# Kernel tuning notes

Hardware: AMD Instinct MI355X
Metric: run time of the kernel (lower is better)

The kernel has to match this reference:

```python
import jax, jax.numpy as jnp
import numpy as np

B, S, H = 4, 512, 768
D, M = 24, 96          # hdim_proj_dim, hdim_mlp_hidden
O = 2 * max(128, H // 2)  # val_mlp hidden = 768


def setup_inputs() -> dict:
    key = jax.random.key(0)
    ks = jax.random.split(key, 14)
    u = lambda k, shp, fan_in: jax.random.uniform(k, shp, jnp.float32, -1.0, 1.0) / np.float32(np.sqrt(fan_in))
    return {
        'H_j': jax.random.normal(ks[0], (B, S, H), jnp.float32),
        'H_i': jax.random.normal(ks[1], (B, S, H), jnp.float32),
        'Wpj': u(ks[2], (H, D), H),
        'Wpi': u(ks[3], (H, D), H),
        'Ws1': u(ks[4], (4 * D, M), 4 * D),
        'bs1': u(ks[5], (M,), 4 * D),
        'ws2': u(ks[6], (M,), M),
        'bs2': u(ks[7], (), M),
        'Wv1': u(ks[8], (3 * H, O), 3 * H),
        'bv1': u(ks[9], (O,), 3 * H),
        'Wv2': u(ks[10], (O, H), O),
        'bv2': u(ks[11], (H,), O),
        'alpha': jnp.float32(0.05),
        'attn_mask': jnp.ones((B, S), jnp.int32),
    }


def reference(H_j, H_i, Wpj, Wpi, Ws1, bs1, ws2, bs2, Wv1, bv1, Wv2, bv2, alpha, attn_mask):
    # Projections [B,S,D]
    Zj = H_j @ Wpj
    Zi = H_i @ Wpi
    # 4term score MLP, first layer decomposed over the concat blocks:
    # cat(Zj_p, Zi_p, Zj_p*Zi_p, |Zj_p - Zi_p|) @ Ws1
    W1j, W1i, W1h, W1d = Ws1[:D], Ws1[D:2 * D], Ws1[2 * D:3 * D], Ws1[3 * D:]
    tj = Zj @ W1j                                   # [B,P,M]
    ti = Zi @ W1i                                   # [B,Q,M]
    th = jnp.einsum('bpd,bqd,dm->bpqm', Zj, Zi, W1h)  # hadamard term
    diff = jnp.abs(Zj[:, :, None, :] - Zi[:, None, :, :])  # [B,P,Q,D]
    td = jnp.einsum('bpqd,dm->bpqm', diff, W1d)
    hid = jax.nn.relu(tj[:, :, None, :] + ti[:, None, :, :] + th + td + bs1)  # [B,P,Q,M]
    logits = jnp.einsum('bpqm,m->bpq', hid, ws2) + bs2  # [B,P,Q]
    # mask over source tokens (last dim); token_temp == 1.0 so no division
    mask = attn_mask.astype(logits.dtype)
    logits = logits + (1.0 - mask)[:, None, :] * jnp.finfo(logits.dtype).min
    probs = jax.nn.softmax(logits, axis=-1)
    ctx = jnp.einsum('bpq,bqh->bph', probs, H_i)    # [B,S,H]
    # val_mlp on cat(ctx, H_j, ctx*H_j), first layer decomposed
    Wc, Wj, Wh = Wv1[:H], Wv1[H:2 * H], Wv1[2 * H:]
    mhid = jax.nn.relu(ctx @ Wc + H_j @ Wj + (ctx * H_j) @ Wh + bv1)
    msg = mhid @ Wv2 + bv2
    # dropout is identity in eval mode
    return alpha * msg
```

## Files before the change

### kernel.cpp

```cpp
#include <hip/hip_runtime.h>
#include <hip/hip_bf16.h>

#define Bb 4
#define Ss 512
#define Hh 768
#define Dd 24
#define Mm 96
#define Oo 768

typedef __bf16 bf16x8 __attribute__((ext_vector_type(8)));
typedef float f32x4 __attribute__((ext_vector_type(4)));

__global__ __launch_bounds__(256) void proj_kernel(
    const float* __restrict__ Hj, const float* __restrict__ Hi,
    const float* __restrict__ Wpj, const float* __restrict__ Wpi,
    float* __restrict__ Zj, float* __restrict__ Zi)
{
    const int row = blockIdx.x;
    const int which = blockIdx.y;
    const float* src = (which ? Hi : Hj) + (size_t)row * Hh;
    const float* W = which ? Wpi : Wpj;
    float* Z = which ? Zi : Zj;
    __shared__ float rowbuf[Hh];
    __shared__ float partial[8][Dd];
    const int tid = threadIdx.x;
    for (int i = tid; i < Hh; i += 256) rowbuf[i] = src[i];
    __syncthreads();
    if (tid < 192) {
        const int d = tid % Dd;
        const int c = tid / Dd;
        const int h0 = c * 96;
        float s = 0.f;
        #pragma unroll 4
        for (int h = h0; h < h0 + 96; ++h) s = fmaf(rowbuf[h], W[h * Dd + d], s);
        partial[c][d] = s;
    }
    __syncthreads();
    if (tid < Dd) {
        float s = 0.f;
        #pragma unroll
        for (int c = 0; c < 8; ++c) s += partial[c][tid];
        Z[(size_t)row * Dd + tid] = s;
    }
}

__global__ __launch_bounds__(256) void transpose_bf16_kernel(
    const float* __restrict__ src, __bf16* __restrict__ dst,
    int R, int C, long sbatch, long dbatch)
{
    const float* s = src + (size_t)blockIdx.z * sbatch;
    __bf16* d = dst + (size_t)blockIdx.z * dbatch;
    __shared__ float t[32][33];
    const int x = threadIdx.x & 31, y = threadIdx.x >> 5;
    const int c0 = blockIdx.x * 32, r0 = blockIdx.y * 32;
    #pragma unroll
    for (int i = 0; i < 4; ++i)
        t[y + 8 * i][x] = s[(size_t)(r0 + y + 8 * i) * C + c0 + x];
    __syncthreads();
    #pragma unroll
    for (int i = 0; i < 4; ++i)
        d[(size_t)(c0 + y + 8 * i) * R + r0 + x] = (__bf16)t[x][y + 8 * i];
}

__global__ __launch_bounds__(256) void hjconv_kernel(
    const float* __restrict__ Hjf, __bf16* __restrict__ Ac)
{
    const int idx = blockIdx.x * 256 + threadIdx.x;
    const int row = idx / 96, c8 = idx % 96;
    const float* s = Hjf + (size_t)row * Hh + c8 * 8;
    const float4 u = *(const float4*)s;
    const float4 v = *(const float4*)(s + 4);
    bf16x8 o;
    o[0]=(__bf16)u.x; o[1]=(__bf16)u.y; o[2]=(__bf16)u.z; o[3]=(__bf16)u.w;
    o[4]=(__bf16)v.x; o[5]=(__bf16)v.y; o[6]=(__bf16)v.z; o[7]=(__bf16)v.w;
    *(bf16x8*)&Ac[(size_t)row * 2304 + Hh + c8 * 8] = o;
}

__global__ __launch_bounds__(256) void wprep_kernel(
    const float* __restrict__ Zj, const float* __restrict__ Ws1,
    const float* __restrict__ bs1, __bf16* __restrict__ Bw)
{
    __shared__ float W[96][97];
    const int tid = threadIdx.x;
    for (int i = tid; i < 96 * 96; i += 256)
        W[i / 96][i % 96] = Ws1[i];
    __syncthreads();
    const int m = tid;
    if (m >= 96) return;
    const float bs1m = bs1[m];
    for (int pp = 0; pp < 8; ++pp) {
        const int p = blockIdx.x * 8 + pp;
        const float* zr = Zj + (size_t)p * Dd;
        float tj = bs1m;
        #pragma unroll
        for (int d = 0; d < Dd; ++d) tj = fmaf(zr[d], W[d][m], tj);
        bf16x8 o[8];
        #pragma unroll
        for (int i = 0; i < 8; ++i) {
            #pragma unroll
            for (int j = 0; j < 8; ++j) {
                const int k = i * 8 + j;
                float v;
                if (k < 24)                 v = fmaf(zr[k], W[48 + k][m], W[24 + k][m]);
                else if (k == 24)           v = tj;
                else if (k >= 32 && k < 56) v = W[72 + (k - 32)][m];
                else                        v = 0.f;
                o[i][j] = (__bf16)v;
            }
        }
        __bf16* dst = Bw + (((size_t)p * 96 + m) << 6);
        #pragma unroll
        for (int i = 0; i < 8; ++i) *(bf16x8*)(dst + i * 8) = o[i];
    }
}

__global__ __launch_bounds__(256) void pair_kernel(
    const float* __restrict__ Zj, const float* __restrict__ Zi,
    const __bf16* __restrict__ Bw, const float* __restrict__ ws2,
    const float* __restrict__ bs2p, const int* __restrict__ mask,
    __bf16* __restrict__ probs)
{
    const int bp = blockIdx.x;
    const int b  = bp >> 9;
    const int tid  = threadIdx.x;
    const int lane = tid & 63;
    const int wid  = tid >> 6;
    const int col  = lane & 15;
    const int g    = lane >> 4;

    __shared__ float logitsl[Ss];
    __shared__ float red[8];

    bf16x8 aw[6][2];
    #pragma unroll
    for (int n = 0; n < 6; ++n) {
        const __bf16* base = Bw + (((size_t)bp * 96 + n * 16 + col) << 6) + g * 8;
        aw[n][0] = *(const bf16x8*)(base);
        aw[n][1] = *(const bf16x8*)(base + 32);
    }
    float ws2r[6][4];
    #pragma unroll
    for (int n = 0; n < 6; ++n) {
        const float4 w4 = *(const float4*)&ws2[n * 16 + g * 4];
        ws2r[n][0] = w4.x; ws2r[n][1] = w4.y; ws2r[n][2] = w4.z; ws2r[n][3] = w4.w;
    }

    float zj8[8];
    if (g < 3) {
        const float* zr = Zj + (size_t)bp * Dd + g * 8;
        const float4 u = *(const float4*)zr;
        const float4 v = *(const float4*)(zr + 4);
        zj8[0]=u.x; zj8[1]=u.y; zj8[2]=u.z; zj8[3]=u.w;
        zj8[4]=v.x; zj8[5]=v.y; zj8[6]=v.z; zj8[7]=v.w;
    } else {
        #pragma unroll
        for (int j = 0; j < 8; ++j) zj8[j] = 0.f;
    }

    const float* zib = Zi + (size_t)b * Ss * Dd;
    const int ko = (g < 3) ? g * 8 : 0;

    float4 cu, cv;
    {
        const float* zr = zib + (size_t)(wid * 128 + col) * Dd + ko;
        cu = *(const float4*)zr; cv = *(const float4*)(zr + 4);
    }

    for (int t = 0; t < 8; ++t) {
        const float4 u = cu, v = cv;
        if (t + 1 < 8) {
            const float* zr = zib + (size_t)(wid * 128 + (t + 1) * 16 + col) * Dd + ko;
            cu = *(const float4*)zr; cv = *(const float4*)(zr + 4);
        }
        bf16x8 b0, b1;
        if (g < 3) {
            b0[0]=(__bf16)u.x; b0[1]=(__bf16)u.y; b0[2]=(__bf16)u.z; b0[3]=(__bf16)u.w;
            b0[4]=(__bf16)v.x; b0[5]=(__bf16)v.y; b0[6]=(__bf16)v.z; b0[7]=(__bf16)v.w;
            b1[0]=(__bf16)fabsf(zj8[0]-u.x); b1[1]=(__bf16)fabsf(zj8[1]-u.y);
            b1[2]=(__bf16)fabsf(zj8[2]-u.z); b1[3]=(__bf16)fabsf(zj8[3]-u.w);
            b1[4]=(__bf16)fabsf(zj8[4]-v.x); b1[5]=(__bf16)fabsf(zj8[5]-v.y);
            b1[6]=(__bf16)fabsf(zj8[6]-v.z); b1[7]=(__bf16)fabsf(zj8[7]-v.w);
        } else {
            #pragma unroll
            for (int j = 0; j < 8; ++j) { b0[j] = (__bf16)0.f; b1[j] = (__bf16)0.f; }
            b0[0] = (__bf16)1.0f;
        }

        f32x4 acc[6];
        #pragma unroll
        for (int n = 0; n < 6; ++n) acc[n] = (f32x4){0.f, 0.f, 0.f, 0.f};
        #pragma unroll
        for (int n = 0; n < 6; ++n) {
            acc[n] = __builtin_amdgcn_mfma_f32_16x16x32_bf16(aw[n][0], b0, acc[n], 0, 0, 0);
            acc[n] = __builtin_amdgcn_mfma_f32_16x16x32_bf16(aw[n][1], b1, acc[n], 0, 0, 0);
        }

        float lsum = 0.f;
        #pragma unroll
        for (int n = 0; n < 6; ++n)
            #pragma unroll
            for (int r = 0; r < 4; ++r)
                lsum = fmaf(fmaxf(acc[n][r], 0.f), ws2r[n][r], lsum);
        lsum += __shfl_xor(lsum, 16);
        lsum += __shfl_xor(lsum, 32);
        if (lane < 16) logitsl[wid * 128 + t * 16 + lane] = lsum;
    }
    __syncthreads();

    const float bs2v = bs2p[0];
    const int* mrow = mask + (size_t)b * Ss;
    float l0 = logitsl[tid]       + bs2v + (1.0f - (float)mrow[tid])       * (-3.402823466e+38f);
    float l1 = logitsl[tid + 256] + bs2v + (1.0f - (float)mrow[tid + 256]) * (-3.402823466e+38f);
    float vmax = fmaxf(l0, l1);
    #pragma unroll
    for (int off = 32; off > 0; off >>= 1) vmax = fmaxf(vmax, __shfl_xor(vmax, off));
    if (lane == 0) red[wid] = vmax;
    __syncthreads();
    const float mx = fmaxf(fmaxf(red[0], red[1]), fmaxf(red[2], red[3]));
    const float e0 = __expf(l0 - mx);
    const float e1 = __expf(l1 - mx);
    float vs = e0 + e1;
    #pragma unroll
    for (int off = 32; off > 0; off >>= 1) vs += __shfl_xor(vs, off);
    if (lane == 0) red[4 + wid] = vs;
    __syncthreads();
    const float inv = 1.0f / (red[4] + red[5] + red[6] + red[7]);
    __bf16* prow = probs + (size_t)bp * Ss;
    prow[tid] = (__bf16)(e0 * inv);
    prow[tid + 256] = (__bf16)(e1 * inv);
}

template<int MODE>
__global__ __launch_bounds__(256) void gemm_kernel(
    const __bf16* __restrict__ A, const __bf16* __restrict__ Bt,
    const float* __restrict__ Hjf, const float* __restrict__ bias,
    const float* __restrict__ alphap,
    __bf16* __restrict__ obf, float* __restrict__ of)
{
    constexpr int K = (MODE == 0) ? 512 : (MODE == 1) ? 2304 : 768;
    constexpr int NIT = K / 64;
    constexpr int LDT = 72;

    __shared__ __bf16 As[64 * LDT];
    __shared__ __bf16 Bs[64 * LDT];

    const int tid = threadIdx.x;
    const int lane = tid & 63;
    const int wid = tid >> 6;
    const int col = lane & 15, g = lane >> 4;
    const int wm = wid >> 1, wn = wid & 1;
    const int r0 = blockIdx.x * 64;
    const int n0 = blockIdx.y * 64;
    const __bf16* Btb = (MODE == 0) ? Bt + (size_t)(r0 >> 9) * (Hh * Ss) : Bt;

    const int srow = tid >> 2;
    const int sc8  = (tid & 3) * 16;
    const __bf16* ag = A   + (size_t)(r0 + srow) * K + sc8;
    const __bf16* bg = Btb + (size_t)(n0 + srow) * K + sc8;
    __bf16* asl = &As[srow * LDT + sc8];
    __bf16* bsl = &Bs[srow * LDT + sc8];

    bf16x8 ra0 = *(const bf16x8*)(ag);
    bf16x8 ra1 = *(const bf16x8*)(ag + 8);
    bf16x8 rb0 = *(const bf16x8*)(bg);
    bf16x8 rb1 = *(const bf16x8*)(bg + 8);

    f32x4 acc[2][2];
    #pragma unroll
    for (int mi = 0; mi < 2; ++mi)
        #pragma unroll
        for (int ni = 0; ni < 2; ++ni) acc[mi][ni] = (f32x4){0.f, 0.f, 0.f, 0.f};

    for (int it = 0; it < NIT; ++it) {
        __syncthreads();
        *(bf16x8*)(asl)     = ra0;
        *(bf16x8*)(asl + 8) = ra1;
        *(bf16x8*)(bsl)     = rb0;
        *(bf16x8*)(bsl + 8) = rb1;
        __syncthreads();
        if (it + 1 < NIT) {
            const int kk = (it + 1) * 64;
            ra0 = *(const bf16x8*)(ag + kk);
            ra1 = *(const bf16x8*)(ag + kk + 8);
            rb0 = *(const bf16x8*)(bg + kk);
            rb1 = *(const bf16x8*)(bg + kk + 8);
        }
        #pragma unroll
        for (int h = 0; h < 2; ++h) {
            bf16x8 a0 = *(const bf16x8*)&As[(wm * 32 + col)      * LDT + h * 32 + g * 8];
            bf16x8 a1 = *(const bf16x8*)&As[(wm * 32 + 16 + col) * LDT + h * 32 + g * 8];
            bf16x8 b0 = *(const bf16x8*)&Bs[(wn * 32 + col)      * LDT + h * 32 + g * 8];
            bf16x8 b1 = *(const bf16x8*)&Bs[(wn * 32 + 16 + col) * LDT + h * 32 + g * 8];
            acc[0][0] = __builtin_amdgcn_mfma_f32_16x16x32_bf16(a0, b0, acc[0][0], 0, 0, 0);
            acc[0][1] = __builtin_amdgcn_mfma_f32_16x16x32_bf16(a0, b1, acc[0][1], 0, 0, 0);
            acc[1][0] = __builtin_amdgcn_mfma_f32_16x16x32_bf16(a1, b0, acc[1][0], 0, 0, 0);
            acc[1][1] = __builtin_amdgcn_mfma_f32_16x16x32_bf16(a1, b1, acc[1][1], 0, 0, 0);
        }
    }

    const float al = (MODE == 2) ? alphap[0] : 0.f;
    #pragma unroll
    for (int mi = 0; mi < 2; ++mi) {
        #pragma unroll
        for (int r = 0; r < 4; ++r) {
            const int row = r0 + wm * 32 + mi * 16 + g * 4 + r;
            #pragma unroll
            for (int ni = 0; ni < 2; ++ni) {
                const int cn = n0 + wn * 32 + ni * 16 + col;
                const float v = acc[mi][ni][r];
                if (MODE == 0) {
                    const float hjv = Hjf[(size_t)row * Hh + cn];
                    obf[(size_t)row * 2304 + cn] = (__bf16)v;
                    obf[(size_t)row * 2304 + 1536 + cn] = (__bf16)(v * hjv);
                } else if (MODE == 1) {
                    obf[(size_t)row * Oo + cn] = (__bf16)fmaxf(v + bias[cn], 0.f);
                } else {
                    of[(size_t)row * Hh + cn] = al * (v + bias[cn]);
                }
            }
        }
    }
}

extern "C" void kernel_launch(void* const* d_in, const int* in_sizes, int n_in,
                              void* d_out, int out_size, void* d_ws, size_t ws_size,
                              hipStream_t stream)
{
    const float* Hj  = (const float*)d_in[0];
    const float* Hi  = (const float*)d_in[1];
    const float* Wpj = (const float*)d_in[2];
    const float* Wpi = (const float*)d_in[3];
    const float* Ws1 = (const float*)d_in[4];
    const float* bs1 = (const float*)d_in[5];
    const float* ws2 = (const float*)d_in[6];
    const float* bs2 = (const float*)d_in[7];
    const float* Wv1 = (const float*)d_in[8];
    const float* bv1 = (const float*)d_in[9];
    const float* Wv2 = (const float*)d_in[10];
    const float* bv2 = (const float*)d_in[11];
    const float* alpha = (const float*)d_in[12];
    const int* mask  = (const int*)d_in[13];

    float* ws = (float*)d_ws;
    float* Zj = ws;
    float* Zi = Zj + 49152;
    float* R0f = Zi + 49152;
    float* R1f = R0f + 524288;
    float* Acat_f = R1f + 786432;
    float* Wv1T_f = Acat_f + 2359296;
    float* Bw_f   = Wv1T_f + 884736;

    __bf16* probs_bf = (__bf16*)R0f;
    __bf16* Wv2T     = (__bf16*)R0f;
    __bf16* HiT      = (__bf16*)R1f;
    __bf16* mhid_bf  = (__bf16*)R1f;
    __bf16* Acat     = (__bf16*)Acat_f;
    __bf16* Wv1T     = (__bf16*)Wv1T_f;
    __bf16* Bw       = (__bf16*)Bw_f;

    proj_kernel<<<dim3(Bb * Ss, 2), 256, 0, stream>>>(Hj, Hi, Wpj, Wpi, Zj, Zi);
    wprep_kernel<<<dim3(256), 256, 0, stream>>>(Zj, Ws1, bs1, Bw);
    transpose_bf16_kernel<<<dim3(Hh / 32, Ss / 32, Bb), 256, 0, stream>>>(
        Hi, HiT, Ss, Hh, (long)Ss * Hh, (long)Hh * Ss);
    transpose_bf16_kernel<<<dim3(Oo / 32, 3 * Hh / 32, 1), 256, 0, stream>>>(
        Wv1, Wv1T, 3 * Hh, Oo, 0, 0);
    hjconv_kernel<<<dim3(768), 256, 0, stream>>>(Hj, Acat);
    pair_kernel<<<dim3(Bb * Ss), 256, 0, stream>>>(Zj, Zi, Bw, ws2, bs2, mask, probs_bf);
    gemm_kernel<0><<<dim3(2048 / 64, Hh / 64), 256, 0, stream>>>(
        probs_bf, HiT, Hj, nullptr, nullptr, Acat, nullptr);
    transpose_bf16_kernel<<<dim3(Hh / 32, Oo / 32, 1), 256, 0, stream>>>(
        Wv2, Wv2T, Oo, Hh, 0, 0);
    gemm_kernel<1><<<dim3(2048 / 64, Oo / 64), 256, 0, stream>>>(
        Acat, Wv1T, nullptr, bv1, nullptr, mhid_bf, nullptr);
    gemm_kernel<2><<<dim3(2048 / 64, Hh / 64), 256, 0, stream>>>(
        mhid_bf, Wv2T, nullptr, bv2, alpha, nullptr, (float*)d_out);
}
```

Baseline: 207.1 us.

## Build pair-kernel MFMA weights in-register instead of materializing per-row Bw

Removes the wprep kernel, which wrote a per-query-row 96x64 bf16 weight tile (about 25 MB) to global memory for pair_kernel to read back. pair_kernel now builds those A operands in registers from a transposed Ws1 (new wst_kernel) and a small per-row tj table (new tj_kernel). Zi is stored padded to 32 columns, with a constant 1 in column 24 for the bias term, so the B-operand construction loses its per-lane branch. This trades a large global write and read for a few extra register FMAs per block and two tiny extra launches.

```diff
diff --git a/kernel.cpp b/kernel.cpp
--- a/kernel.cpp
+++ b/kernel.cpp
@@ -14,13 +14,12 @@
 __global__ __launch_bounds__(256) void proj_kernel(
     const float* __restrict__ Hj, const float* __restrict__ Hi,
     const float* __restrict__ Wpj, const float* __restrict__ Wpi,
-    float* __restrict__ Zj, float* __restrict__ Zi)
+    float* __restrict__ Zj, float* __restrict__ Zip)
 {
     const int row = blockIdx.x;
     const int which = blockIdx.y;
     const float* src = (which ? Hi : Hj) + (size_t)row * Hh;
     const float* W = which ? Wpi : Wpj;
-    float* Z = which ? Zi : Zj;
     __shared__ float rowbuf[Hh];
     __shared__ float partial[8][Dd];
     const int tid = threadIdx.x;
@@ -40,26 +39,33 @@
         float s = 0.f;
         #pragma unroll
         for (int c = 0; c < 8; ++c) s += partial[c][tid];
-        Z[(size_t)row * Dd + tid] = s;
-    }
-}
-
-__global__ __launch_bounds__(256) void transpose_bf16_kernel(
-    const float* __restrict__ src, __bf16* __restrict__ dst,
-    int R, int C, long sbatch, long dbatch)
-{
-    const float* s = src + (size_t)blockIdx.z * sbatch;
-    __bf16* d = dst + (size_t)blockIdx.z * dbatch;
-    __shared__ float t[32][33];
-    const int x = threadIdx.x & 31, y = threadIdx.x >> 5;
-    const int c0 = blockIdx.x * 32, r0 = blockIdx.y * 32;
-    #pragma unroll
-    for (int i = 0; i < 4; ++i)
-        t[y + 8 * i][x] = s[(size_t)(r0 + y + 8 * i) * C + c0 + x];
-    __syncthreads();
-    #pragma unroll
-    for (int i = 0; i < 4; ++i)
-        d[(size_t)(c0 + y + 8 * i) * R + r0 + x] = (__bf16)t[x][y + 8 * i];
+        if (which) Zip[(size_t)row * 32 + tid] = s;
+        else       Zj[(size_t)row * Dd + tid] = s;
+    }
+    if (which && tid >= Dd && tid < 32)
+        Zip[(size_t)row * 32 + tid] = (tid == 24) ? 1.0f : 0.0f;
+}
+
+__global__ __launch_bounds__(256) void wst_kernel(
+    const float* __restrict__ Ws1, float* __restrict__ WsT)
+{
+    __shared__ float W[96][97];
+    for (int i = threadIdx.x; i < 96 * 96; i += 256) W[i / 96][i % 96] = Ws1[i];
+    __syncthreads();
+    for (int i = threadIdx.x; i < 96 * 96; i += 256) WsT[i] = W[i % 96][i / 96];
+}
+
+__global__ __launch_bounds__(256) void tj_kernel(
+    const float* __restrict__ Zj, const float* __restrict__ Ws1,
+    const float* __restrict__ bs1, float* __restrict__ tj_all)
+{
+    const int idx = blockIdx.x * 256 + threadIdx.x;
+    const int p = idx / 96, m = idx % 96;
+    float s = bs1[m];
+    const float* zr = Zj + (size_t)p * Dd;
+    #pragma unroll
+    for (int d = 0; d < Dd; ++d) s = fmaf(zr[d], Ws1[d * Mm + m], s);
+    tj_all[idx] = s;
 }
 
 __global__ __launch_bounds__(256) void hjconv_kernel(
@@ -76,49 +82,29 @@
     *(bf16x8*)&Ac[(size_t)row * 2304 + Hh + c8 * 8] = o;
 }
 
-__global__ __launch_bounds__(256) void wprep_kernel(
-    const float* __restrict__ Zj, const float* __restrict__ Ws1,
-    const float* __restrict__ bs1, __bf16* __restrict__ Bw)
-{
-    __shared__ float W[96][97];
-    const int tid = threadIdx.x;
-    for (int i = tid; i < 96 * 96; i += 256)
-        W[i / 96][i % 96] = Ws1[i];
-    __syncthreads();
-    const int m = tid;
-    if (m >= 96) return;
-    const float bs1m = bs1[m];
-    for (int pp = 0; pp < 8; ++pp) {
-        const int p = blockIdx.x * 8 + pp;
-        const float* zr = Zj + (size_t)p * Dd;
-        float tj = bs1m;
-        #pragma unroll
-        for (int d = 0; d < Dd; ++d) tj = fmaf(zr[d], W[d][m], tj);
-        bf16x8 o[8];
-        #pragma unroll
-        for (int i = 0; i < 8; ++i) {
-            #pragma unroll
-            for (int j = 0; j < 8; ++j) {
-                const int k = i * 8 + j;
-                float v;
-                if (k < 24)                 v = fmaf(zr[k], W[48 + k][m], W[24 + k][m]);
-                else if (k == 24)           v = tj;
-                else if (k >= 32 && k < 56) v = W[72 + (k - 32)][m];
-                else                        v = 0.f;
-                o[i][j] = (__bf16)v;
-            }
-        }
-        __bf16* dst = Bw + (((size_t)p * 96 + m) << 6);
-        #pragma unroll
-        for (int i = 0; i < 8; ++i) *(bf16x8*)(dst + i * 8) = o[i];
-    }
+__global__ __launch_bounds__(256) void transpose_bf16_kernel(
+    const float* __restrict__ src, __bf16* __restrict__ dst,
+    int R, int C, long sbatch, long dbatch)
+{
+    const float* s = src + (size_t)blockIdx.z * sbatch;
+    __bf16* d = dst + (size_t)blockIdx.z * dbatch;
+    __shared__ float t[32][33];
+    const int x = threadIdx.x & 31, y = threadIdx.x >> 5;
+    const int c0 = blockIdx.x * 32, r0 = blockIdx.y * 32;
+    #pragma unroll
+    for (int i = 0; i < 4; ++i)
+        t[y + 8 * i][x] = s[(size_t)(r0 + y + 8 * i) * C + c0 + x];
+    __syncthreads();
+    #pragma unroll
+    for (int i = 0; i < 4; ++i)
+        d[(size_t)(c0 + y + 8 * i) * R + r0 + x] = (__bf16)t[x][y + 8 * i];
 }
 
 __global__ __launch_bounds__(256) void pair_kernel(
-    const float* __restrict__ Zj, const float* __restrict__ Zi,
-    const __bf16* __restrict__ Bw, const float* __restrict__ ws2,
-    const float* __restrict__ bs2p, const int* __restrict__ mask,
-    __bf16* __restrict__ probs)
+    const float* __restrict__ Zj, const float* __restrict__ Zip,
+    const float* __restrict__ WsT, const float* __restrict__ tj_all,
+    const float* __restrict__ ws2, const float* __restrict__ bs2p,
+    const int* __restrict__ mask, __bf16* __restrict__ probs)
 {
     const int bp = blockIdx.x;
     const int b  = bp >> 9;
@@ -131,20 +117,7 @@
     __shared__ float logitsl[Ss];
     __shared__ float red[8];
 
-    bf16x8 aw[6][2];
-    #pragma unroll
-    for (int n = 0; n < 6; ++n) {
-        const __bf16* base = Bw + (((size_t)bp * 96 + n * 16 + col) << 6) + g * 8;
-        aw[n][0] = *(const bf16x8*)(base);
-        aw[n][1] = *(const bf16x8*)(base + 32);
-    }
-    float ws2r[6][4];
-    #pragma unroll
-    for (int n = 0; n < 6; ++n) {
-        const float4 w4 = *(const float4*)&ws2[n * 16 + g * 4];
-        ws2r[n][0] = w4.x; ws2r[n][1] = w4.y; ws2r[n][2] = w4.z; ws2r[n][3] = w4.w;
-    }
-
+    const float km = (g < 3) ? 1.0f : 0.0f;
     float zj8[8];
     if (g < 3) {
         const float* zr = Zj + (size_t)bp * Dd + g * 8;
@@ -157,34 +130,54 @@
         for (int j = 0; j < 8; ++j) zj8[j] = 0.f;
     }
 
-    const float* zib = Zi + (size_t)b * Ss * Dd;
-    const int ko = (g < 3) ? g * 8 : 0;
+    bf16x8 aw[6][2];
+    float ws2r[6][4];
+    #pragma unroll
+    for (int n = 0; n < 6; ++n) {
+        const int m = n * 16 + col;
+        const float4 w4 = *(const float4*)&ws2[n * 16 + g * 4];
+        ws2r[n][0] = w4.x; ws2r[n][1] = w4.y; ws2r[n][2] = w4.z; ws2r[n][3] = w4.w;
+        bf16x8 a0, a1;
+        if (g < 3) {
+            const float* wr = WsT + (size_t)m * 96;
+            const float4 i0 = *(const float4*)(wr + 24 + g * 8);
+            const float4 i1 = *(const float4*)(wr + 28 + g * 8);
+            const float4 h0 = *(const float4*)(wr + 48 + g * 8);
+            const float4 h1 = *(const float4*)(wr + 52 + g * 8);
+            const float4 d0 = *(const float4*)(wr + 72 + g * 8);
+            const float4 d1 = *(const float4*)(wr + 76 + g * 8);
+            a0[0]=(__bf16)fmaf(zj8[0], h0.x, i0.x); a0[1]=(__bf16)fmaf(zj8[1], h0.y, i0.y);
+            a0[2]=(__bf16)fmaf(zj8[2], h0.z, i0.z); a0[3]=(__bf16)fmaf(zj8[3], h0.w, i0.w);
+            a0[4]=(__bf16)fmaf(zj8[4], h1.x, i1.x); a0[5]=(__bf16)fmaf(zj8[5], h1.y, i1.y);
+            a0[6]=(__bf16)fmaf(zj8[6], h1.z, i1.z); a0[7]=(__bf16)fmaf(zj8[7], h1.w, i1.w);
+            a1[0]=(__bf16)d0.x; a1[1]=(__bf16)d0.y; a1[2]=(__bf16)d0.z; a1[3]=(__bf16)d0.w;
+            a1[4]=(__bf16)d1.x; a1[5]=(__bf16)d1.y; a1[6]=(__bf16)d1.z; a1[7]=(__bf16)d1.w;
+        } else {
+            #pragma unroll
+            for (int j = 0; j < 8; ++j) { a0[j] = (__bf16)0.f; a1[j] = (__bf16)0.f; }
+            a0[0] = (__bf16)tj_all[(size_t)bp * 96 + m];
+        }
+        aw[n][0] = a0; aw[n][1] = a1;
+    }
+
+    const float* zb = Zip + ((size_t)(b * Ss + wid * 128 + col) * 32) + g * 8;
 
     float4 cu, cv;
-    {
-        const float* zr = zib + (size_t)(wid * 128 + col) * Dd + ko;
-        cu = *(const float4*)zr; cv = *(const float4*)(zr + 4);
-    }
+    cu = *(const float4*)zb; cv = *(const float4*)(zb + 4);
 
     for (int t = 0; t < 8; ++t) {
         const float4 u = cu, v = cv;
         if (t + 1 < 8) {
-            const float* zr = zib + (size_t)(wid * 128 + (t + 1) * 16 + col) * Dd + ko;
+            const float* zr = zb + (size_t)(t + 1) * 16 * 32;
             cu = *(const float4*)zr; cv = *(const float4*)(zr + 4);
         }
         bf16x8 b0, b1;
-        if (g < 3) {
-            b0[0]=(__bf16)u.x; b0[1]=(__bf16)u.y; b0[2]=(__bf16)u.z; b0[3]=(__bf16)u.w;
-            b0[4]=(__bf16)v.x; b0[5]=(__bf16)v.y; b0[6]=(__bf16)v.z; b0[7]=(__bf16)v.w;
-            b1[0]=(__bf16)fabsf(zj8[0]-u.x); b1[1]=(__bf16)fabsf(zj8[1]-u.y);
-            b1[2]=(__bf16)fabsf(zj8[2]-u.z); b1[3]=(__bf16)fabsf(zj8[3]-u.w);
-            b1[4]=(__bf16)fabsf(zj8[4]-v.x); b1[5]=(__bf16)fabsf(zj8[5]-v.y);
-            b1[6]=(__bf16)fabsf(zj8[6]-v.z); b1[7]=(__bf16)fabsf(zj8[7]-v.w);
-        } else {
-            #pragma unroll
-            for (int j = 0; j < 8; ++j) { b0[j] = (__bf16)0.f; b1[j] = (__bf16)0.f; }
-            b0[0] = (__bf16)1.0f;
-        }
+        b0[0]=(__bf16)u.x; b0[1]=(__bf16)u.y; b0[2]=(__bf16)u.z; b0[3]=(__bf16)u.w;
+        b0[4]=(__bf16)v.x; b0[5]=(__bf16)v.y; b0[6]=(__bf16)v.z; b0[7]=(__bf16)v.w;
+        b1[0]=(__bf16)(fabsf(zj8[0]-u.x)*km); b1[1]=(__bf16)(fabsf(zj8[1]-u.y)*km);
+        b1[2]=(__bf16)(fabsf(zj8[2]-u.z)*km); b1[3]=(__bf16)(fabsf(zj8[3]-u.w)*km);
+        b1[4]=(__bf16)(fabsf(zj8[4]-v.x)*km); b1[5]=(__bf16)(fabsf(zj8[5]-v.y)*km);
+        b1[6]=(__bf16)(fabsf(zj8[6]-v.z)*km); b1[7]=(__bf16)(fabsf(zj8[7]-v.w)*km);
 
         f32x4 acc[6];
         #pragma unroll
@@ -342,13 +335,14 @@
     const int* mask  = (const int*)d_in[13];
 
     float* ws = (float*)d_ws;
-    float* Zj = ws;
-    float* Zi = Zj + 49152;
-    float* R0f = Zi + 49152;
-    float* R1f = R0f + 524288;
+    float* Zj     = ws;
+    float* Zip    = Zj + 49152;
+    float* WsT    = Zip + 65536;
+    float* tj_all = WsT + 9216;
+    float* R0f    = tj_all + 196608;
+    float* R1f    = R0f + 524288;
     float* Acat_f = R1f + 786432;
     float* Wv1T_f = Acat_f + 2359296;
-    float* Bw_f   = Wv1T_f + 884736;
 
     __bf16* probs_bf = (__bf16*)R0f;
     __bf16* Wv2T     = (__bf16*)R0f;
@@ -356,16 +350,17 @@
     __bf16* mhid_bf  = (__bf16*)R1f;
     __bf16* Acat     = (__bf16*)Acat_f;
     __bf16* Wv1T     = (__bf16*)Wv1T_f;
-    __bf16* Bw       = (__bf16*)Bw_f;
-
-    proj_kernel<<<dim3(Bb * Ss, 2), 256, 0, stream>>>(Hj, Hi, Wpj, Wpi, Zj, Zi);
-    wprep_kernel<<<dim3(256), 256, 0, stream>>>(Zj, Ws1, bs1, Bw);
+
+    proj_kernel<<<dim3(Bb * Ss, 2), 256, 0, stream>>>(Hj, Hi, Wpj, Wpi, Zj, Zip);
+    wst_kernel<<<dim3(1), 256, 0, stream>>>(Ws1, WsT);
+    tj_kernel<<<dim3(768), 256, 0, stream>>>(Zj, Ws1, bs1, tj_all);
     transpose_bf16_kernel<<<dim3(Hh / 32, Ss / 32, Bb), 256, 0, stream>>>(
         Hi, HiT, Ss, Hh, (long)Ss * Hh, (long)Hh * Ss);
     transpose_bf16_kernel<<<dim3(Oo / 32, 3 * Hh / 32, 1), 256, 0, stream>>>(
         Wv1, Wv1T, 3 * Hh, Oo, 0, 0);
     hjconv_kernel<<<dim3(768), 256, 0, stream>>>(Hj, Acat);
-    pair_kernel<<<dim3(Bb * Ss), 256, 0, stream>>>(Zj, Zi, Bw, ws2, bs2, mask, probs_bf);
+    pair_kernel<<<dim3(Bb * Ss), 256, 0, stream>>>(
+        Zj, Zip, WsT, tj_all, ws2, bs2, mask, probs_bf);
     gemm_kernel<0><<<dim3(2048 / 64, Hh / 64), 256, 0, stream>>>(
         probs_bf, HiT, Hj, nullptr, nullptr, Acat, nullptr);
     transpose_bf16_kernel<<<dim3(Hh / 32, Oo / 32, 1), 256, 0, stream>>>(
```

Result: slower. 212.3 us (+2.5%).
